# Performance work log

Hardware: AMD Instinct MI355X
Metric: run time of the kernel (lower is better)

## Reference

```python
import jax, jax.numpy as jnp
import numpy as np

INPUT_DIM = 8192
HIDDEN = 512
EMBED = HIDDEN // 2  # op embedding dim
NUM_TEMPERS = 64
NUM_OPS = 3
MAX_HOPS = 4
B = 2048


def setup_inputs() -> dict:
    key = jax.random.key(0)
    ks = jax.random.split(key, 10)
    n = lambda k, shape: jax.random.normal(k, shape, jnp.float32)
    return {
        "x": n(ks[0], (B, INPUT_DIM)),
        "op_emb": 0.01 * n(ks[1], (NUM_OPS, EMBED)),
        "op_logits": jnp.zeros((NUM_OPS,), jnp.float32),
        "id_embeds": 0.01 * n(ks[2], (128, 4)),
        "W1": n(ks[3], (HIDDEN + 4 + EMBED, HIDDEN)) / np.sqrt(HIDDEN + 4 + EMBED),
        "b1": jnp.zeros((HIDDEN,), jnp.float32),
        "W2": n(ks[4], (HIDDEN, HIDDEN)) / np.sqrt(HIDDEN),
        "b2": jnp.zeros((HIDDEN,), jnp.float32),
        "Wr1": n(ks[5], (HIDDEN + 4, 32)) / np.sqrt(HIDDEN + 4),
        "br1": jnp.zeros((32,), jnp.float32),
        "Wr2": n(ks[6], (32, NUM_TEMPERS + 1)) / np.sqrt(32),
        "br2": jnp.zeros((NUM_TEMPERS + 1,), jnp.float32),
        "Wp": n(ks[7], (HIDDEN, INPUT_DIM)) / np.sqrt(HIDDEN),
        "bp": jnp.zeros((INPUT_DIM,), jnp.float32),
        "tid_emb": 0.01 * n(ks[8], (NUM_TEMPERS, 4)),
        "rng_seed": 42,
    }


def reference(x, op_emb, op_logits, id_embeds, W1, b1, W2, b2, Wr1, br1, Wr2, br2, Wp, bp, tid_emb, rng_seed):
    Bx, D = x.shape
    # D is a multiple of HIDDEN here -> no padding branch needed
    num_patches = D // HIDDEN
    patch_states = x.reshape(Bx * num_patches, HIDDEN)
    N = patch_states.shape[0]

    rng = jax.random.key(rng_seed)
    rng, tk = jax.random.split(rng)
    patch_tempers = jax.random.randint(tk, (N,), 0, NUM_TEMPERS)
    patch_done = jnp.zeros((N,), bool)

    # Fixed-length unroll of the while_loop (max_hops=4). Early-exit only
    # differs if ALL patches stop early, which is vanishingly unlikely.
    for hop in range(MAX_HOPS):
        # --- gather active patches (inactive slots fill with index 0, as in original) ---
        active_idx = jnp.where(~patch_done, size=N, fill_value=0)[0]
        x_active = patch_states[active_idx]          # [N, HIDDEN]
        t_active = patch_tempers[active_idx]         # [N]
        # --- Temper: sample op per patch, embed, 2-layer relu MLP ---
        rng, ok = jax.random.split(rng)
        op_probs = jax.nn.softmax(op_logits)
        op_idx = jax.random.categorical(ok, jnp.log(op_probs), shape=(N,))
        x_aug = jnp.concatenate([x_active, id_embeds[t_active], op_emb[op_idx]], axis=-1)
        h = jax.nn.relu(x_aug @ W1 + b1)
        h = jax.nn.relu(h @ W2 + b2)                 # [N, HIDDEN]
        # --- scatter back updated states ---
        patch_states = patch_states.at[active_idx].set(h)
        # --- routing policy + categorical sampling of next temper / stop ---
        enriched = jnp.concatenate([h, tid_emb[t_active]], axis=-1)
        logits = jax.nn.relu(enriched @ Wr1 + br1) @ Wr2 + br2
        rng, sk = jax.random.split(rng)
        sampled = jax.random.categorical(sk, jax.nn.log_softmax(logits))
        stop = sampled == NUM_TEMPERS
        next_t = jnp.clip(sampled, 0, NUM_TEMPERS - 1)
        patch_tempers = patch_tempers.at[active_idx].set(next_t)
        patch_done = patch_done.at[active_idx].set(stop)

    latent = patch_states.reshape(Bx, num_patches, HIDDEN).mean(axis=1)  # [B, HIDDEN]
    pred = latent @ Wp + bp                                              # [B, INPUT_DIM]
    return latent, pred
```

## Files before the change

kernel.cpp:

```cpp
#include <hip/hip_runtime.h>
#include <cstdint>
#include <cstddef>


#define NPATCH 32768
#define NHOP 4
#define RSCALE 4096.0f
#define RINV   2.44140625e-4f

typedef unsigned short u16;
typedef __attribute__((ext_vector_type(8))) _Float16 half8;
typedef __attribute__((ext_vector_type(4))) float f32x4;

#define GLDS(gp, lp) __builtin_amdgcn_global_load_lds( \
    (const __attribute__((address_space(1))) void*)(const void*)(gp), \
    (__attribute__((address_space(3))) void*)(void*)(lp), 16, 0, 0)

__device__ __forceinline__ uint32_t rotl32(uint32_t x, int r){ return (x<<r)|(x>>(32-r)); }

__device__ __forceinline__ void tf2x32(uint32_t k0, uint32_t k1, uint32_t x0, uint32_t x1,
                                       uint32_t& o0, uint32_t& o1){
  uint32_t k2 = k0 ^ k1 ^ 0x1BD11BDAu;
  x0 += k0; x1 += k1;
#define TFR(r) { x0 += x1; x1 = rotl32(x1,(r)); x1 ^= x0; }
  TFR(13) TFR(15) TFR(26) TFR(6)   x0 += k1; x1 += k2 + 1u;
  TFR(17) TFR(29) TFR(16) TFR(24)  x0 += k2; x1 += k0 + 2u;
  TFR(13) TFR(15) TFR(26) TFR(6)   x0 += k0; x1 += k1 + 3u;
  TFR(17) TFR(29) TFR(16) TFR(24)  x0 += k1; x1 += k2 + 4u;
  TFR(13) TFR(15) TFR(26) TFR(6)   x0 += k2; x1 += k0 + 5u;
#undef TFR
  o0 = x0; o1 = x1;
}

__device__ __forceinline__ uint32_t jbits32(uint32_t k0, uint32_t k1, uint32_t idx){
  uint32_t a, b; tf2x32(k0, k1, 0u, idx, a, b);
  return a ^ b;
}

__device__ __forceinline__ void jsplit(uint32_t& r0, uint32_t& r1, uint32_t& c0, uint32_t& c1){
  uint32_t n0, n1;
  tf2x32(r0, r1, 0u, 0u, n0, n1);
  tf2x32(r0, r1, 0u, 1u, c0, c1);
  r0 = n0; r1 = n1;
}

__device__ __forceinline__ float jgumbel(uint32_t bits){
  float f = __uint_as_float(0x3f800000u | (bits >> 9)) - 1.0f;
  float u = fmaxf(f, 1.17549435e-38f);
  return -logf(-logf(u));
}

union uhcv { _Float16 h; u16 u; };
__device__ __forceinline__ u16 f2h(float x){ uhcv t; t.h = (_Float16)x; return t.u; }
__device__ __forceinline__ float h2f(u16 b){ uhcv t; t.u = b; return (float)t.h; }
__device__ __forceinline__ void split2s(float v, u16& a0, u16& a1){
  a0 = f2h(v);
  a1 = f2h((v - h2f(a0)) * RSCALE);
}

__global__ void k_keys(const int* __restrict__ seed, const float* __restrict__ op_logits,
                       uint32_t* __restrict__ keys, float* __restrict__ logp3){
  if (threadIdx.x != 0 || blockIdx.x != 0) return;
  uint32_t r0 = 0u, r1 = (uint32_t)seed[0];
  uint32_t c0, c1;
  jsplit(r0, r1, c0, c1); keys[0] = c0; keys[1] = c1;
  for (int h = 0; h < NHOP; h++){
    jsplit(r0, r1, c0, c1); keys[2 + 4*h] = c0; keys[3 + 4*h] = c1;
    jsplit(r0, r1, c0, c1); keys[4 + 4*h] = c0; keys[5 + 4*h] = c1;
  }
  float l0 = op_logits[0], l1 = op_logits[1], l2 = op_logits[2];
  float mm = fmaxf(l0, fmaxf(l1, l2));
  float e0 = expf(l0-mm), e1 = expf(l1-mm), e2 = expf(l2-mm);
  float ssum = e0 + e1 + e2;
  logp3[0] = logf(e0/ssum); logp3[1] = logf(e1/ssum); logp3[2] = logf(e2/ssum);
}

__global__ __launch_bounds__(256)
void k_init(const uint32_t* __restrict__ keys, int* __restrict__ tempers, int* __restrict__ done){
  int i = blockIdx.x*256 + threadIdx.x;
  uint32_t b = jbits32(keys[0], keys[1], (uint32_t)(NPATCH + i));
  tempers[i] = (int)(b & 63u);
  done[i] = 0;
}

__global__ __launch_bounds__(256)
void k_precomp(const float* __restrict__ id_embeds, const float* __restrict__ op_emb,
               const float* __restrict__ tid_emb,
               const float* __restrict__ W1, const float* __restrict__ b1,
               const float* __restrict__ Wr1, const float* __restrict__ br1,
               float* __restrict__ idW, float* __restrict__ opWb, float* __restrict__ tidWb){
  int b = blockIdx.x, tid = threadIdx.x;
  if (b < 64){
    for (int j = tid; j < 512; j += 256){
      float v = 0.f;
      #pragma unroll
      for (int u = 0; u < 4; u++) v = fmaf(id_embeds[b*4+u], W1[(size_t)(512+u)*512 + j], v);
      idW[b*512 + j] = v;
    }
  } else if (b < 67){
    int o = b - 64;
    for (int j = tid; j < 512; j += 256){
      float v = b1[j];
      for (int u = 0; u < 256; u++) v = fmaf(op_emb[o*256+u], W1[(size_t)(516+u)*512 + j], v);
      opWb[o*512 + j] = v;
    }
  } else {
    for (int idx = tid; idx < 2048; idx += 256){
      int t = idx >> 5, c = idx & 31;
      float v = br1[c];
      #pragma unroll
      for (int u = 0; u < 4; u++) v = fmaf(tid_emb[t*4+u], Wr1[(512+u)*32 + c], v);
      tidWb[idx] = v;
    }
  }
}

__global__ __launch_bounds__(256)
void k_splitW(const float* __restrict__ W1, const float* __restrict__ W2,
              const float* __restrict__ Wp, const float* __restrict__ Wr1,
              u16* __restrict__ W1T, u16* __restrict__ W2T, u16* __restrict__ WpT,
              u16* __restrict__ Wr1P){
  __shared__ float t[32][33];
  int blk = blockIdx.x;
  const float* src; u16* dst; int N; int deg; size_t pst; int tb;
  if (blk < 256){ src = W1; dst = W1T; N = 512; deg = 2; pst = (size_t)512*512; tb = blk; }
  else if (blk < 512){ src = W2; dst = W2T; N = 512; deg = 2; pst = (size_t)512*512; tb = blk - 256; }
  else if (blk < 528){ src = Wr1; dst = Wr1P; N = 32; deg = 2; pst = (size_t)32*512; tb = blk - 512; }
  else { src = Wp; dst = WpT; N = 8192; deg = 1; pst = 0; tb = blk - 528; }
  int n0 = (tb >> 4)*32, k0 = (tb & 15)*32;
  if (N == 32){ n0 = 0; k0 = tb*32; }
  int r = threadIdx.x >> 5, c = threadIdx.x & 31;
  for (int rr = r; rr < 32; rr += 8)
    t[rr][c] = src[(size_t)(k0+rr)*N + ((n0 + c) % N)];
  __syncthreads();
  for (int rr = r; rr < 32; rr += 8){
    if (n0 + rr >= N) break;
    float v = t[c][rr];
    size_t o = (size_t)(n0+rr)*512 + k0 + c;
    if (deg == 2){
      u16 a0, a1; split2s(v, a0, a1);
      dst[o] = a0; dst[pst + o] = a1;
    } else {
      dst[o] = f2h(v);
    }
  }
}

__global__ __launch_bounds__(256)
void k_xsplit(const float* __restrict__ x, u16* __restrict__ sP){
  size_t i = ((size_t)blockIdx.x*256 + threadIdx.x)*4;
  float4 v = *(const float4*)(x + i);
  ushort4 p0, p1;
  split2s(v.x, p0.x, p1.x); split2s(v.y, p0.y, p1.y);
  split2s(v.z, p0.z, p1.z); split2s(v.w, p0.w, p1.w);
  const size_t SP = (size_t)NPATCH*512;
  *(ushort4*)(sP + i) = p0; *(ushort4*)(sP + SP + i) = p1;
}

__global__ __launch_bounds__(1024)
void k_scan1(const int* __restrict__ done, int* __restrict__ lpref,
             int* __restrict__ partials){
  __shared__ int cnt[1024];
  const int tid = threadIdx.x;
  const int e = blockIdx.x*1024 + tid;
  int f = (done[e] == 0);
  cnt[tid] = f;
  __syncthreads();
  int val = f;
  for (int off = 1; off < 1024; off <<= 1){
    int v = (tid >= off) ? cnt[tid - off] : 0;
    __syncthreads();
    val += v; cnt[tid] = val;
    __syncthreads();
  }
  lpref[e] = val - f;
  if (tid == 1023) partials[blockIdx.x] = val;
}

__global__ __launch_bounds__(1024)
void k_scan3(const int* __restrict__ done, const int* __restrict__ lpref,
             const int* __restrict__ partials,
             const int* __restrict__ tempers,
             const uint32_t* __restrict__ keys, const float* __restrict__ logp3,
             int hop, int* __restrict__ aidx, int* __restrict__ t_act,
             int* __restrict__ op_idx, int* __restrict__ meta){
  __shared__ int sb[33];
  const int tid = threadIdx.x;
  if (tid < 64){
    int f = (tid < 32) ? partials[tid] : 0;
    int v = f;
    #pragma unroll
    for (int off = 1; off < 32; off <<= 1){
      int u = __shfl_up(v, off);
      if (tid >= off) v += u;
    }
    if (tid < 32) sb[tid] = v - f;
    if (tid == 31) sb[32] = v;
  }
  __syncthreads();
  const int base = sb[blockIdx.x];
  const int na = sb[32];
  const int e = blockIdx.x*1024 + tid;
  const int lp = lpref[e];
  const int f = (done[e] == 0);
  const int pos = f ? (base + lp) : (na + (e - base - lp));
  const int p = f ? e : 0;
  aidx[pos] = p;
  t_act[pos] = tempers[p];
  const uint32_t k0 = keys[2 + 4*hop], k1 = keys[3 + 4*hop];
  float best = 0.f; int bi = 0;
  #pragma unroll
  for (int c = 0; c < 3; c++){
    float v = jgumbel(jbits32(k0, k1, (uint32_t)(3*pos + c))) + logp3[c];
    if (c == 0 || v > best){ best = v; bi = c; }
  }
  op_idx[pos] = bi;
  if (blockIdx.x == 0 && tid == 0){
    meta[0] = na;
    meta[1] = (na < NPATCH) ? (NPATCH - 1) : 0;
  }
}

__global__ __launch_bounds__(1024)
void k_scan(const int* __restrict__ done, int* __restrict__ aidx, int* __restrict__ meta){
  __shared__ int cnt[1024];
  int tid = threadIdx.x;
  int base = tid * 32;
  unsigned flags = 0; int c = 0;
  #pragma unroll
  for (int i = 0; i < 32; i++){
    int f = (done[base + i] == 0);
    flags |= ((unsigned)f) << i;
    c += f;
  }
  cnt[tid] = c;
  __syncthreads();
  int val = c;
  for (int off = 1; off < 1024; off <<= 1){
    int v = (tid >= off) ? cnt[tid - off] : 0;
    __syncthreads();
    val += v; cnt[tid] = val;
    __syncthreads();
  }
  int pos = val - c;
  for (int i = 0; i < 32; i++){
    if ((flags >> i) & 1u) aidx[pos++] = base + i;
  }
  __syncthreads();
  int na = cnt[1023];
  for (int j = na + tid; j < NPATCH; j += 1024) aidx[j] = 0;
  if (tid == 0){
    meta[0] = na;
    meta[1] = (na < NPATCH) ? (NPATCH - 1) : 0;
  }
}

__global__ __launch_bounds__(256)
void k_gather(const int* __restrict__ aidx, const int* __restrict__ tempers,
              const uint32_t* __restrict__ keys, const float* __restrict__ logp3,
              int hop, int* __restrict__ t_act, int* __restrict__ op_idx){
  int s = blockIdx.x*256 + threadIdx.x;
  int p = aidx[s];
  t_act[s] = tempers[p];
  uint32_t k0 = keys[2 + 4*hop], k1 = keys[3 + 4*hop];
  float best = 0.f; int bi = 0;
  #pragma unroll
  for (int c = 0; c < 3; c++){
    float v = jgumbel(jbits32(k0, k1, (uint32_t)(3*s + c))) + logp3[c];
    if (c == 0 || v > best){ best = v; bi = c; }
  }
  op_idx[s] = bi;
}

template<int MODE, int DEG>
__global__ __launch_bounds__(256, 2)
void k_mgemm(const u16* __restrict__ Ap, const u16* __restrict__ Bp,
             float* __restrict__ outF, u16* __restrict__ outP,
             const int* __restrict__ aidx, const float* __restrict__ bias,
             const float* __restrict__ idW, const float* __restrict__ opWb,
             const int* __restrict__ t_act, const int* __restrict__ op_idx,
             const int* __restrict__ meta,
             int Ncols, size_t aStride, size_t bStride, size_t oStride){
  __shared__ u16 As[2*DEG*4096];
  __shared__ u16 Bs[2*DEG*4096];
  const int tid = threadIdx.x;
  const int L = tid & 63, w = tid >> 6;

  const int gx = (int)gridDim.x;
  const int nwg = gx * (int)gridDim.y;
  int lin = (int)blockIdx.y * gx + (int)blockIdx.x;
  if ((nwg & 7) == 0)
    lin = (lin & 7) * (nwg >> 3) + (lin >> 3);
  const int m0 = (lin / gx) * 128, n0 = (lin % gx) * 128;
  const int wr = w >> 1, wc = w & 1;

  constexpr int SPW = DEG*4;
  constexpr int BUFO = DEG*4096;
  const bool isA = (w < 2);
  const u16* gB = isA ? Ap : Bp;
  u16* lB = isA ? As : Bs;
  const size_t pstride = isA ? aStride : bStride;
  const u16* gseg[8];
  u16* lseg[8];
  #pragma unroll
  for (int q = 0; q < SPW; q++){
    int ss = (w & 1)*SPW + q;
    int p = ss >> 3, rb = ss & 7;
    int row16 = rb*16 + (L >> 2);
    int grow;
    if (isA) grow = (MODE == 1) ? aidx[m0 + row16] : (m0 + row16);
    else     grow = n0 + row16;
    int swz = (L & 3) ^ ((L >> 2) & 3);
    gseg[q] = gB + p*pstride + (size_t)grow*512 + swz*8;
    lseg[q] = lB + p*4096 + rb*512;
  }

  f32x4 accM[4][4], accR[4][4];
  #pragma unroll
  for (int i = 0; i < 4; i++)
    #pragma unroll
    for (int j = 0; j < 4; j++){ accM[i][j] = (f32x4)0.f; accR[i][j] = (f32x4)0.f; }

  const int rdsw = ((L >> 4) ^ (L & 3))*8;
  const int frow = L & 15;

  #pragma unroll
  for (int q = 0; q < SPW; q++)
    GLDS(gseg[q], lseg[q]);

  #pragma unroll 2
  for (int kt = 0; kt < 16; kt++){
    const int cb = (kt & 1) * BUFO;
    if (kt < 15){
      const int nb = ((kt + 1) & 1) * BUFO;
      #pragma unroll
      for (int q = 0; q < SPW; q++)
        GLDS(gseg[q] + (kt+1)*32, lseg[q] + nb);
      asm volatile("s_waitcnt vmcnt(%0)" :: "n"(SPW) : "memory");
    } else {
      asm volatile("s_waitcnt vmcnt(0)" ::: "memory");
    }
    __builtin_amdgcn_s_barrier();
    asm volatile("" ::: "memory");

    __builtin_amdgcn_s_setprio(1);
    half8 af[DEG][4], bf[DEG][4];
    #pragma unroll
    for (int pa = 0; pa < DEG; pa++)
      #pragma unroll
      for (int i = 0; i < 4; i++)
        af[pa][i] = *(const half8*)&As[cb + pa*4096 + (wr*64 + i*16 + frow)*32 + rdsw];
    #pragma unroll
    for (int pb = 0; pb < DEG; pb++)
      #pragma unroll
      for (int j = 0; j < 4; j++)
        bf[pb][j] = *(const half8*)&Bs[cb + pb*4096 + (wc*64 + j*16 + frow)*32 + rdsw];
    #pragma unroll
    for (int pa = 0; pa < DEG; pa++)
      #pragma unroll
      for (int pb = 0; pb < DEG - pa; pb++)
        #pragma unroll
        for (int j = 0; j < 4; j++)
          #pragma unroll
          for (int i = 0; i < 4; i++){
            if (pa + pb == 0)
              accM[i][j] = __builtin_amdgcn_mfma_f32_16x16x32_f16(af[0][i], bf[0][j], accM[i][j], 0, 0, 0);
            else
              accR[i][j] = __builtin_amdgcn_mfma_f32_16x16x32_f16(af[pa][i], bf[pb][j], accR[i][j], 0, 0, 0);
          }
    __builtin_amdgcn_s_setprio(0);

    asm volatile("" ::: "memory");
    __builtin_amdgcn_s_barrier();
  }

  const int rbase = m0 + wr*64 + (L >> 4)*4;
  const int cbase = n0 + wc*64 + (L & 15);
  const int w0v = (MODE == 3) ? meta[1] : 0;
  #pragma unroll
  for (int i = 0; i < 4; i++){
    #pragma unroll
    for (int reg = 0; reg < 4; reg++){
      int r = rbase + i*16 + reg;
      if (MODE == 1){
        int t = t_act[r], o = op_idx[r];
        #pragma unroll
        for (int j = 0; j < 4; j++){
          int c = cbase + j*16;
          float v = accM[i][j][reg] + RINV*accR[i][j][reg] + idW[t*512 + c] + opWb[o*512 + c];
          v = fmaxf(v, 0.f);
          u16 a0, a1; split2s(v, a0, a1);
          size_t off = (size_t)r*512 + c;
          outP[off] = a0; outP[oStride + off] = a1;
        }
      } else if (MODE == 3){
        int p = aidx[r];
        bool allowed = (p != 0) || (r == w0v);
        #pragma unroll
        for (int j = 0; j < 4; j++){
          int c = cbase + j*16;
          float v = accM[i][j][reg] + RINV*accR[i][j][reg] + bias[c];
          v = fmaxf(v, 0.f);
          if (allowed){
            u16 a0, a1; split2s(v, a0, a1);
            size_t off = (size_t)p*512 + c;
            outP[off] = a0; outP[oStride + off] = a1;
          }
        }
      } else {
        #pragma unroll
        for (int j = 0; j < 4; j++){
          int c = cbase + j*16;
          float v = accM[i][j][reg] + bias[c];
          if (DEG == 2) v += RINV*accR[i][j][reg];
          outF[(size_t)r*Ncols + c] = v;
        }
      }
    }
  }
}

__global__ __launch_bounds__(256)
void k_routemm(const u16* __restrict__ sP, const u16* __restrict__ Wr1P,
               const int* __restrict__ aidx, const int* __restrict__ t_act,
               const float* __restrict__ tidWb,
               const float* __restrict__ Wr2, const float* __restrict__ br2,
               const int* __restrict__ meta, const uint32_t* __restrict__ keys,
               int hop, int* __restrict__ tempers, int* __restrict__ done){
  __shared__ float l32s[64][32];
  __shared__ float Wr2s[32*65];
  const int tid = threadIdx.x;
  const int L = tid & 63, w = tid >> 6;
  const int s0 = blockIdx.x*64 + w*16;
  const size_t SPh = (size_t)NPATCH*512;

  for (int i = tid; i < 32*65; i += 256) Wr2s[i] = Wr2[i];

  const int arow = aidx[s0 + (L & 15)];
  const u16* a0p = sP + (size_t)arow*512 + (L >> 4)*8;
  const u16* a1p = a0p + SPh;
  const u16* bb = Wr1P + (size_t)(L & 15)*512 + (L >> 4)*8;
  const size_t BPL = (size_t)32*512;
  const size_t BCT = (size_t)16*512;

  f32x4 accM[2], accR[2];
  accM[0] = (f32x4)0.f; accM[1] = (f32x4)0.f;
  accR[0] = (f32x4)0.f; accR[1] = (f32x4)0.f;

  #pragma unroll 4
  for (int kt = 0; kt < 16; kt++){
    const int ko = kt*32;
    half8 a0  = *(const half8*)(a0p + ko);
    half8 a1  = *(const half8*)(a1p + ko);
    half8 b00 = *(const half8*)(bb + ko);
    half8 b01 = *(const half8*)(bb + BCT + ko);
    half8 b10 = *(const half8*)(bb + BPL + ko);
    half8 b11 = *(const half8*)(bb + BPL + BCT + ko);
    accM[0] = __builtin_amdgcn_mfma_f32_16x16x32_f16(a0, b00, accM[0], 0, 0, 0);
    accM[1] = __builtin_amdgcn_mfma_f32_16x16x32_f16(a0, b01, accM[1], 0, 0, 0);
    accR[0] = __builtin_amdgcn_mfma_f32_16x16x32_f16(a0, b10, accR[0], 0, 0, 0);
    accR[1] = __builtin_amdgcn_mfma_f32_16x16x32_f16(a0, b11, accR[1], 0, 0, 0);
    accR[0] = __builtin_amdgcn_mfma_f32_16x16x32_f16(a1, b00, accR[0], 0, 0, 0);
    accR[1] = __builtin_amdgcn_mfma_f32_16x16x32_f16(a1, b01, accR[1], 0, 0, 0);
  }

  #pragma unroll
  for (int reg = 0; reg < 4; reg++){
    int sl = w*16 + (L >> 4)*4 + reg;
    int s = blockIdx.x*64 + sl;
    int t = t_act[s];
    #pragma unroll
    for (int ct = 0; ct < 2; ct++){
      int c = ct*16 + (L & 15);
      float v = accM[ct][reg] + RINV*accR[ct][reg] + tidWb[t*32 + c];
      l32s[sl][c] = fmaxf(v, 0.f);
    }
  }
  __syncthreads();

  const uint32_t sk0 = keys[4 + 4*hop], sk1 = keys[5 + 4*hop];
  const int w0v = meta[1];
  for (int rr = 0; rr < 16; rr++){
    const int sl = w*16 + rr;
    const int ps = blockIdx.x*64 + sl;
    const int c = L;
    float lg = br2[c];
    #pragma unroll
    for (int k = 0; k < 32; k++) lg = fmaf(l32s[sl][k], Wr2s[k*65 + c], lg);
    float lg64 = br2[64];
    #pragma unroll
    for (int k = 0; k < 32; k++) lg64 = fmaf(l32s[sl][k], Wr2s[k*65 + 64], lg64);
    float m = lg;
    for (int off = 32; off; off >>= 1) m = fmaxf(m, __shfl_xor(m, off));
    m = fmaxf(m, lg64);
    float se = expf(lg - m);
    for (int off = 32; off; off >>= 1) se += __shfl_xor(se, off);
    se += expf(lg64 - m);
    float Lse = logf(se);
    float g = jgumbel(jbits32(sk0, sk1, (uint32_t)(65*ps + c)));
    float v = (lg - m) - Lse + g;
    int idx = c;
    for (int off = 32; off; off >>= 1){
      float ov = __shfl_xor(v, off);
      int   oi = __shfl_xor(idx, off);
      if (ov > v || (ov == v && oi < idx)){ v = ov; idx = oi; }
    }
    float g64 = jgumbel(jbits32(sk0, sk1, (uint32_t)(65*ps + 64)));
    float v64 = (lg64 - m) - Lse + g64;
    if (v64 > v) idx = 64;
    if (L == 0){
      const int p = aidx[ps];
      const bool allowed = (p != 0) || (ps == w0v);
      if (allowed){
        tempers[p] = (idx < 63) ? idx : 63;
        done[p]    = (idx == 64) ? 1 : 0;
      }
    }
  }
}

__global__ __launch_bounds__(256)
void k_latent2(const u16* __restrict__ sP, float* __restrict__ outF, u16* __restrict__ latP){
  int idx = blockIdx.x*256 + threadIdx.x;
  int b = idx >> 7, j4 = (idx & 127)*4;
  const size_t SP = (size_t)NPATCH*512;
  float s0 = 0.f, s1 = 0.f, s2 = 0.f, s3 = 0.f;
  #pragma unroll 4
  for (int u = 0; u < 16; u++){
    size_t e = (size_t)(b*16 + u)*512 + j4;
    ushort4 v0 = *(const ushort4*)(sP + e);
    ushort4 v1 = *(const ushort4*)(sP + SP + e);
    s0 += h2f(v0.x) + RINV*h2f(v1.x);
    s1 += h2f(v0.y) + RINV*h2f(v1.y);
    s2 += h2f(v0.z) + RINV*h2f(v1.z);
    s3 += h2f(v0.w) + RINV*h2f(v1.w);
  }
  s0 *= 0.0625f; s1 *= 0.0625f; s2 *= 0.0625f; s3 *= 0.0625f;
  float4 fo; fo.x = s0; fo.y = s1; fo.z = s2; fo.w = s3;
  *(float4*)(outF + (size_t)b*512 + j4) = fo;
  ushort4 lp; lp.x = f2h(s0); lp.y = f2h(s1); lp.z = f2h(s2); lp.w = f2h(s3);
  *(ushort4*)(latP + (size_t)b*512 + j4) = lp;
}

template<int MODE>
__global__ __launch_bounds__(256)
void k_gemmF(const float* __restrict__ A, const float* __restrict__ B, float* __restrict__ C,
             int Ncols,
             const int* __restrict__ aidx,
             const float* __restrict__ bias,
             const float* __restrict__ idW, const float* __restrict__ opWb,
             const int* __restrict__ t_act, const int* __restrict__ op_idx){
  __shared__ float As[16][128];
  __shared__ float Bs[16][128];
  const int tid = threadIdx.x;
  const int bx = blockIdx.x, by = blockIdx.y;
  const int tx = tid & 15, ty = tid >> 4;
  const int lr = tid >> 1, lhalf = tid & 1;
  const int srow = by*128 + lr;
  const int arow = (MODE == 1) ? aidx[srow] : srow;
  const float* Ap = A + (size_t)arow*512 + lhalf*8;
  const float* Bp = B + (size_t)(tid >> 4)*Ncols + bx*128 + (tid & 15)*8;

  float acc[8][8];
  #pragma unroll
  for (int i = 0; i < 8; i++)
    #pragma unroll
    for (int j = 0; j < 8; j++) acc[i][j] = 0.f;

  for (int kt = 0; kt < 512; kt += 16){
    float4 a0 = *(const float4*)(Ap + kt);
    float4 a1 = *(const float4*)(Ap + kt + 4);
    float4 g0 = *(const float4*)(Bp + (size_t)kt*Ncols);
    float4 g1 = *(const float4*)(Bp + (size_t)kt*Ncols + 4);
    __syncthreads();
    As[lhalf*8+0][lr] = a0.x; As[lhalf*8+1][lr] = a0.y;
    As[lhalf*8+2][lr] = a0.z; As[lhalf*8+3][lr] = a0.w;
    As[lhalf*8+4][lr] = a1.x; As[lhalf*8+5][lr] = a1.y;
    As[lhalf*8+6][lr] = a1.z; As[lhalf*8+7][lr] = a1.w;
    *(float4*)&Bs[tid>>4][(tid&15)*8]     = g0;
    *(float4*)&Bs[tid>>4][(tid&15)*8 + 4] = g1;
    __syncthreads();
    #pragma unroll
    for (int k = 0; k < 16; k++){
      float4 av0 = *(float4*)&As[k][ty*8];
      float4 av1 = *(float4*)&As[k][ty*8+4];
      float4 bv0 = *(float4*)&Bs[k][tx*4];
      float4 bv1 = *(float4*)&Bs[k][64 + tx*4];
      float av[8] = {av0.x,av0.y,av0.z,av0.w,av1.x,av1.y,av1.z,av1.w};
      float bv[8] = {bv0.x,bv0.y,bv0.z,bv0.w,bv1.x,bv1.y,bv1.z,bv1.w};
      #pragma unroll
      for (int i = 0; i < 8; i++)
        #pragma unroll
        for (int j = 0; j < 8; j++)
          acc[i][j] = fmaf(av[i], bv[j], acc[i][j]);
    }
  }

  const int col0a = bx*128 + tx*4;
  const int col0b = col0a + 64;
  #pragma unroll
  for (int i = 0; i < 8; i++){
    int s = by*128 + ty*8 + i;
    float adda[4], addb[4];
    if (MODE == 1){
      int t = t_act[s], o = op_idx[s];
      float4 ia = *(const float4*)&idW[t*512 + col0a];
      float4 ib = *(const float4*)&idW[t*512 + col0b];
      float4 oa = *(const float4*)&opWb[o*512 + col0a];
      float4 ob = *(const float4*)&opWb[o*512 + col0b];
      adda[0]=ia.x+oa.x; adda[1]=ia.y+oa.y; adda[2]=ia.z+oa.z; adda[3]=ia.w+oa.w;
      addb[0]=ib.x+ob.x; addb[1]=ib.y+ob.y; addb[2]=ib.z+ob.z; addb[3]=ib.w+ob.w;
    } else {
      float4 ba = *(const float4*)&bias[col0a];
      float4 bb = *(const float4*)&bias[col0b];
      adda[0]=ba.x; adda[1]=ba.y; adda[2]=ba.z; adda[3]=ba.w;
      addb[0]=bb.x; addb[1]=bb.y; addb[2]=bb.z; addb[3]=bb.w;
    }
    float4 va, vb;
    float* pa = &va.x; float* pb = &vb.x;
    #pragma unroll
    for (int j = 0; j < 4; j++){
      float v0 = acc[i][j]   + adda[j];
      float v1 = acc[i][j+4] + addb[j];
      if (MODE != 2){ v0 = fmaxf(v0, 0.f); v1 = fmaxf(v1, 0.f); }
      pa[j] = v0; pb[j] = v1;
    }
    *(float4*)(C + (size_t)s*Ncols + col0a) = va;
    *(float4*)(C + (size_t)s*Ncols + col0b) = vb;
  }
}

__global__ __launch_bounds__(256)
void k_routeF(const float* __restrict__ h2, const float* __restrict__ Wr1,
              const float* __restrict__ Wr2, const float* __restrict__ br2,
              const float* __restrict__ tidWb,
              const int* __restrict__ t_act, const int* __restrict__ aidx,
              const int* __restrict__ meta, const uint32_t* __restrict__ keys, int hop,
              float* __restrict__ states, int* __restrict__ tempers, int* __restrict__ done){
  __shared__ float Wr1s[256][32];
  __shared__ float h2s[8][512];
  __shared__ float l32[8][32];

  const int tid = threadIdx.x;
  const int s0 = blockIdx.x * 8;

  for (int i4 = tid; i4 < 8*128; i4 += 256){
    int sl = i4 >> 7, q = i4 & 127;
    *(float4*)&h2s[sl][q*4] = *(const float4*)&h2[(size_t)(s0+sl)*512 + q*4];
  }

  const int lane = tid & 63, w = tid >> 6;
  const int half = lane >> 5, col = lane & 31;
  const int sl = w*2 + half;
  const int s  = s0 + sl;
  const int t  = t_act[s];
  float acc = tidWb[t*32 + col];

  for (int kh = 0; kh < 2; kh++){
    __syncthreads();
    for (int idx = tid; idx < 256*32; idx += 256)
      Wr1s[idx >> 5][idx & 31] = Wr1[kh*8192 + idx];
    __syncthreads();
    const int kb = kh * 256;
    #pragma unroll 4
    for (int k4 = 0; k4 < 64; k4++){
      float4 hv = *(float4*)&h2s[sl][kb + k4*4];
      acc = fmaf(hv.x, Wr1s[k4*4+0][col], acc);
      acc = fmaf(hv.y, Wr1s[k4*4+1][col], acc);
      acc = fmaf(hv.z, Wr1s[k4*4+2][col], acc);
      acc = fmaf(hv.w, Wr1s[k4*4+3][col], acc);
    }
  }
  l32[sl][col] = fmaxf(acc, 0.f);
  __syncthreads();

  const uint32_t sk0 = keys[4 + 4*hop], sk1 = keys[5 + 4*hop];
  int smp[2];
  for (int pass = 0; pass < 2; pass++){
    const int psl = w*2 + pass;
    const int ps  = s0 + psl;
    const int c = lane;
    float lg = br2[c];
    #pragma unroll
    for (int k = 0; k < 32; k++) lg = fmaf(l32[psl][k], Wr2[k*65 + c], lg);
    float lg64 = br2[64];
    #pragma unroll
    for (int k = 0; k < 32; k++) lg64 = fmaf(l32[psl][k], Wr2[k*65 + 64], lg64);
    float m = lg;
    for (int off = 32; off; off >>= 1) m = fmaxf(m, __shfl_xor(m, off));
    m = fmaxf(m, lg64);
    float se = expf(lg - m);
    for (int off = 32; off; off >>= 1) se += __shfl_xor(se, off);
    se += expf(lg64 - m);
    float Lse = logf(se);
    float g = jgumbel(jbits32(sk0, sk1, (uint32_t)(65*ps + c)));
    float v = (lg - m) - Lse + g;
    int idx = c;
    for (int off = 32; off; off >>= 1){
      float ov = __shfl_xor(v, off);
      int   oi = __shfl_xor(idx, off);
      if (ov > v || (ov == v && oi < idx)){ v = ov; idx = oi; }
    }
    float g64 = jgumbel(jbits32(sk0, sk1, (uint32_t)(65*ps + 64)));
    float v64 = (lg64 - m) - Lse + g64;
    if (v64 > v) idx = 64;
    smp[pass] = idx;
  }

  const int mysmp = smp[half];
  const int p = aidx[s];
  const int w0v = meta[1];
  const bool allowed = (p != 0) || (s == w0v);
  if (allowed){
    const float4* src = (const float4*)&h2s[sl][0];
    float4* dst = (float4*)(states + (size_t)p*512);
    for (int q = col; q < 128; q += 32) dst[q] = src[q];
    if (col == 0){
      tempers[p] = (mysmp < 63) ? mysmp : 63;
      done[p]    = (mysmp == 64) ? 1 : 0;
    }
  }
}

__global__ __launch_bounds__(256)
void k_latentF(const float* __restrict__ states, float* __restrict__ out){
  int idx = blockIdx.x*256 + threadIdx.x;
  int b = idx >> 9, j = idx & 511;
  float s = 0.f;
  #pragma unroll
  for (int u = 0; u < 16; u++) s += states[(size_t)(b*16 + u)*512 + j];
  out[idx] = s * 0.0625f;
}

extern "C" void kernel_launch(void* const* d_in, const int* in_sizes, int n_in,
                              void* d_out, int out_size, void* d_ws, size_t ws_size,
                              hipStream_t stream) {
  (void)in_sizes; (void)n_in; (void)out_size;
  const float* x         = (const float*)d_in[0];
  const float* op_emb    = (const float*)d_in[1];
  const float* op_logits = (const float*)d_in[2];
  const float* id_embeds = (const float*)d_in[3];
  const float* W1        = (const float*)d_in[4];
  const float* b1        = (const float*)d_in[5];
  const float* W2        = (const float*)d_in[6];
  const float* b2        = (const float*)d_in[7];
  const float* Wr1       = (const float*)d_in[8];
  const float* br1       = (const float*)d_in[9];
  const float* Wr2       = (const float*)d_in[10];
  const float* br2       = (const float*)d_in[11];
  const float* Wp        = (const float*)d_in[12];
  const float* bp        = (const float*)d_in[13];
  const float* tid_emb   = (const float*)d_in[14];
  const int*   seed      = (const int*)d_in[15];
  float* out = (float*)d_out;

  char* w = (char*)d_ws;
  uint32_t* keys = (uint32_t*)w;
  float* logp3   = (float*)(w + 256);
  int*   meta    = (int*)(w + 512);
  int*   tempers = (int*)(w + 4096);
  int*   done    = tempers + NPATCH;
  int*   t_act   = done + NPATCH;
  int*   op_idx  = t_act + NPATCH;
  int*   aidx    = op_idx + NPATCH;
  int*   lpref   = aidx + NPATCH;
  float* idW     = (float*)(lpref + NPATCH);
  float* opWb    = idW + 64*512;
  float* tidWb   = opWb + 3*512;
  int*   partials= (int*)(tidWb + 2048);

  const size_t SPh = (size_t)NPATCH*512;
  u16* W1T     = (u16*)(w + (1u<<20));
  u16* W2T     = W1T + (size_t)2*512*512;
  u16* Wr1P    = W2T + (size_t)2*512*512;
  u16* WpT     = Wr1P + (size_t)2*32*512;
  u16* latP    = WpT + (size_t)8192*512;
  u16* statesP = latP + (size_t)2048*512;
  u16* h1P     = statesP + 2*SPh;
  const size_t NEED = (size_t)((char*)(h1P + 2*SPh) - w);

  k_keys<<<1, 64, 0, stream>>>(seed, op_logits, keys, logp3);
  k_init<<<NPATCH/256, 256, 0, stream>>>(keys, tempers, done);
  k_precomp<<<68, 256, 0, stream>>>(id_embeds, op_emb, tid_emb, W1, b1, Wr1, br1,
                                    idW, opWb, tidWb);

  if (ws_size >= NEED){
    k_splitW<<<4624, 256, 0, stream>>>(W1, W2, Wp, Wr1, W1T, W2T, WpT, Wr1P);
    k_xsplit<<<(NPATCH*512/4)/256, 256, 0, stream>>>(x, statesP);

    for (int hop = 0; hop < NHOP; hop++){
      k_scan1<<<NPATCH/1024, 1024, 0, stream>>>(done, lpref, partials);
      k_scan3<<<NPATCH/1024, 1024, 0, stream>>>(done, lpref, partials,
                                                tempers, keys, logp3, hop,
                                                aidx, t_act, op_idx, meta);
      k_mgemm<1,2><<<dim3(4, NPATCH/128), 256, 0, stream>>>(
          statesP, W1T, nullptr, h1P, aidx, nullptr, idW, opWb, t_act, op_idx, meta,
          512, SPh, (size_t)512*512, SPh);
      k_mgemm<3,2><<<dim3(4, NPATCH/128), 256, 0, stream>>>(
          h1P, W2T, nullptr, statesP, aidx, b2, nullptr, nullptr, nullptr, nullptr, meta,
          512, SPh, (size_t)512*512, SPh);
      k_routemm<<<NPATCH/64, 256, 0, stream>>>(statesP, Wr1P, aidx, t_act, tidWb,
                                               Wr2, br2, meta, keys, hop,
                                               tempers, done);
    }

    k_latent2<<<(2048*512/4)/256, 256, 0, stream>>>(statesP, out, latP);
    k_mgemm<2,1><<<dim3(64, 16), 256, 0, stream>>>(
        latP, WpT, out + 2048*512, nullptr, nullptr, bp, nullptr, nullptr, nullptr, nullptr,
        nullptr, 8192, (size_t)2048*512, (size_t)8192*512, 0);
  } else {
    const size_t BIG0 = 2u<<20;
    const size_t SB   = (size_t)NPATCH * 512 * sizeof(float);
    float *states, *h1, *h2;
    bool copy_states;
    if (ws_size >= BIG0 + 3*SB){
      states = (float*)(w + BIG0);
      h1     = (float*)(w + BIG0 + SB);
      h2     = (float*)(w + BIG0 + 2*SB);
      copy_states = true;
    } else {
      states = (float*)d_in[0];
      h1     = (float*)(w + BIG0);
      h2     = (float*)(w + BIG0 + SB);
      copy_states = false;
    }
    if (copy_states)
      hipMemcpyAsync(states, x, SB, hipMemcpyDeviceToDevice, stream);

    for (int hop = 0; hop < NHOP; hop++){
      k_scan<<<1, 1024, 0, stream>>>(done, aidx, meta);
      k_gather<<<NPATCH/256, 256, 0, stream>>>(aidx, tempers, keys, logp3, hop, t_act, op_idx);
      k_gemmF<1><<<dim3(4, NPATCH/128), 256, 0, stream>>>(states, W1, h1, 512,
                                      aidx, nullptr, idW, opWb, t_act, op_idx);
      k_gemmF<0><<<dim3(4, NPATCH/128), 256, 0, stream>>>(h1, W2, h2, 512,
                                      nullptr, b2, nullptr, nullptr, nullptr, nullptr);
      k_routeF<<<NPATCH/8, 256, 0, stream>>>(h2, Wr1, Wr2, br2, tidWb, t_act, aidx,
                                      meta, keys, hop, states, tempers, done);
    }

    k_latentF<<<(2048*512)/256, 256, 0, stream>>>(states, out);
    k_gemmF<2><<<dim3(8192/128, 2048/128), 256, 0, stream>>>(out, Wp, out + 2048*512, 8192,
                                      nullptr, bp, nullptr, nullptr, nullptr, nullptr);
  }
}
```

Before: 986.0 us.

## Add split-precision GEMM kernel with four-slot half-tile LDS pipeline

Adds a dedicated k_mgemmP kernel for the two per-hop split-fp16 GEMMs. It stages the high and low halves of each K tile into separate LDS slots in a four-deep ring, so loads of the next half overlap with MFMAs on the current one, with a barrier at each half-step. It also restructures fragment reads in the remaining generic k_mgemm to load B fragments per column, reducing register pressure. The aim is to hide global-to-LDS latency and raise MFMA utilisation, at the cost of more barriers and hand-tuned vmcnt waits that must stay matched to the number of loads issued.

```diff
diff --git a/kernel.cpp b/kernel.cpp
--- a/kernel.cpp
+++ b/kernel.cpp
@@ -272,6 +272,157 @@
   op_idx[s] = bi;
 }
 
+template<int MODE>
+__global__ __launch_bounds__(256, 2)
+void k_mgemmP(const u16* __restrict__ Ap, const u16* __restrict__ Bp,
+              u16* __restrict__ outP,
+              const int* __restrict__ aidx, const float* __restrict__ bias,
+              const float* __restrict__ idW, const float* __restrict__ opWb,
+              const int* __restrict__ t_act, const int* __restrict__ op_idx,
+              const int* __restrict__ meta,
+              size_t aStride, size_t bStride, size_t oStride){
+  __shared__ u16 As[4*4096];
+  __shared__ u16 Bs[4*4096];
+  const int tid = threadIdx.x;
+  const int L = tid & 63, w = tid >> 6;
+
+  const int gx = (int)gridDim.x;
+  const int nwg = gx * (int)gridDim.y;
+  int lin = (int)blockIdx.y * gx + (int)blockIdx.x;
+  if ((nwg & 7) == 0)
+    lin = (lin & 7) * (nwg >> 3) + (lin >> 3);
+  const int m0 = (lin / gx) * 128, n0 = (lin % gx) * 128;
+  const int wr = w >> 1, wc = w & 1;
+
+  const int swz = (L & 3) ^ ((L >> 2) & 3);
+  const int row16 = L >> 2;
+  const u16* gA[2][2];
+  const u16* gB[2][2];
+  int lofs[2];
+  #pragma unroll
+  for (int q = 0; q < 2; q++){
+    const int rb = 2*w + q;
+    lofs[q] = rb*512;
+    int growA = m0 + rb*16 + row16;
+    if (MODE == 1) growA = aidx[growA];
+    const int growB = n0 + rb*16 + row16;
+    #pragma unroll
+    for (int p = 0; p < 2; p++){
+      gA[p][q] = Ap + p*aStride + (size_t)growA*512 + swz*8;
+      gB[p][q] = Bp + p*bStride + (size_t)growB*512 + swz*8;
+    }
+  }
+
+#define ISSUE_HALF(t, p) { const int _sl = ((2*(t)+(p)) & 3)*4096; \
+    GLDS(gA[p][0] + (t)*32, As + _sl + lofs[0]); \
+    GLDS(gA[p][1] + (t)*32, As + _sl + lofs[1]); \
+    GLDS(gB[p][0] + (t)*32, Bs + _sl + lofs[0]); \
+    GLDS(gB[p][1] + (t)*32, Bs + _sl + lofs[1]); }
+
+  f32x4 accM[4][4], accR[4][4];
+  #pragma unroll
+  for (int i = 0; i < 4; i++)
+    #pragma unroll
+    for (int j = 0; j < 4; j++){ accM[i][j] = (f32x4)0.f; accR[i][j] = (f32x4)0.f; }
+
+  const int rdsw = ((L >> 4) ^ (L & 3))*8;
+  const int frow = L & 15;
+
+#define READ_FRAGS(dA, dB, sl) { \
+    const int _b = (sl)*4096; \
+    dA[0] = *(const half8*)&As[_b + (wr*64 +  0 + frow)*32 + rdsw]; \
+    dA[1] = *(const half8*)&As[_b + (wr*64 + 16 + frow)*32 + rdsw]; \
+    dA[2] = *(const half8*)&As[_b + (wr*64 + 32 + frow)*32 + rdsw]; \
+    dA[3] = *(const half8*)&As[_b + (wr*64 + 48 + frow)*32 + rdsw]; \
+    dB[0] = *(const half8*)&Bs[_b + (wc*64 +  0 + frow)*32 + rdsw]; \
+    dB[1] = *(const half8*)&Bs[_b + (wc*64 + 16 + frow)*32 + rdsw]; \
+    dB[2] = *(const half8*)&Bs[_b + (wc*64 + 32 + frow)*32 + rdsw]; \
+    dB[3] = *(const half8*)&Bs[_b + (wc*64 + 48 + frow)*32 + rdsw]; }
+
+#define MFMA_CL(dst, aa, bb) { \
+    _Pragma("unroll") \
+    for (int j = 0; j < 4; j++) \
+      _Pragma("unroll") \
+      for (int i = 0; i < 4; i++) \
+        dst[i][j] = __builtin_amdgcn_mfma_f32_16x16x32_f16(aa[i], bb[j], dst[i][j], 0, 0, 0); }
+
+  ISSUE_HALF(0, 0); ISSUE_HALF(0, 1); ISSUE_HALF(1, 0);
+
+  half8 af0[4], bf0[4], af1[4], bf1[4];
+
+  for (int t = 0; t < 15; t++){
+    asm volatile("s_waitcnt vmcnt(8)" ::: "memory");
+    __builtin_amdgcn_s_barrier();
+    asm volatile("" ::: "memory");
+    ISSUE_HALF(t+1, 1);
+    READ_FRAGS(af0, bf0, (2*t) & 3);
+    __builtin_amdgcn_s_setprio(1);
+    MFMA_CL(accM, af0, bf0);
+    __builtin_amdgcn_s_setprio(0);
+    asm volatile("s_waitcnt vmcnt(8)" ::: "memory");
+    __builtin_amdgcn_s_barrier();
+    asm volatile("" ::: "memory");
+    if (t < 14) ISSUE_HALF(t+2, 0);
+    READ_FRAGS(af1, bf1, (2*t+1) & 3);
+    __builtin_amdgcn_s_setprio(1);
+    MFMA_CL(accR, af0, bf1);
+    MFMA_CL(accR, af1, bf0);
+    __builtin_amdgcn_s_setprio(0);
+  }
+  asm volatile("s_waitcnt vmcnt(4)" ::: "memory");
+  __builtin_amdgcn_s_barrier();
+  asm volatile("" ::: "memory");
+  READ_FRAGS(af0, bf0, 2);
+  MFMA_CL(accM, af0, bf0);
+  asm volatile("s_waitcnt vmcnt(0)" ::: "memory");
+  __builtin_amdgcn_s_barrier();
+  asm volatile("" ::: "memory");
+  READ_FRAGS(af1, bf1, 3);
+  MFMA_CL(accR, af0, bf1);
+  MFMA_CL(accR, af1, bf0);
+
+#undef ISSUE_HALF
+#undef READ_FRAGS
+#undef MFMA_CL
+
+  const int rbase = m0 + wr*64 + (L >> 4)*4;
+  const int cbase = n0 + wc*64 + (L & 15);
+  const int w0v = (MODE == 3) ? meta[1] : 0;
+  #pragma unroll
+  for (int i = 0; i < 4; i++){
+    #pragma unroll
+    for (int reg = 0; reg < 4; reg++){
+      int r = rbase + i*16 + reg;
+      if (MODE == 1){
+        int t = t_act[r], o = op_idx[r];
+        #pragma unroll
+        for (int j = 0; j < 4; j++){
+          int c = cbase + j*16;
+          float v = accM[i][j][reg] + RINV*accR[i][j][reg] + idW[t*512 + c] + opWb[o*512 + c];
+          v = fmaxf(v, 0.f);
+          u16 a0, a1; split2s(v, a0, a1);
+          size_t off = (size_t)r*512 + c;
+          outP[off] = a0; outP[oStride + off] = a1;
+        }
+      } else {
+        int p = aidx[r];
+        bool allowed = (p != 0) || (r == w0v);
+        #pragma unroll
+        for (int j = 0; j < 4; j++){
+          int c = cbase + j*16;
+          float v = accM[i][j][reg] + RINV*accR[i][j][reg] + bias[c];
+          v = fmaxf(v, 0.f);
+          if (allowed){
+            u16 a0, a1; split2s(v, a0, a1);
+            size_t off = (size_t)p*512 + c;
+            outP[off] = a0; outP[oStride + off] = a1;
+          }
+        }
+      }
+    }
+  }
+}
+
 template<int MODE, int DEG>
 __global__ __launch_bounds__(256, 2)
 void k_mgemm(const u16* __restrict__ Ap, const u16* __restrict__ Bp,
@@ -344,30 +495,27 @@
     asm volatile("" ::: "memory");
 
     __builtin_amdgcn_s_setprio(1);
-    half8 af[DEG][4], bf[DEG][4];
-    #pragma unroll
-    for (int pa = 0; pa < DEG; pa++)
+    #pragma unroll
+    for (int pa = 0; pa < DEG; pa++){
+      half8 af[4];
       #pragma unroll
       for (int i = 0; i < 4; i++)
-        af[pa][i] = *(const half8*)&As[cb + pa*4096 + (wr*64 + i*16 + frow)*32 + rdsw];
-    #pragma unroll
-    for (int pb = 0; pb < DEG; pb++)
+        af[i] = *(const half8*)&As[cb + pa*4096 + (wr*64 + i*16 + frow)*32 + rdsw];
       #pragma unroll
-      for (int j = 0; j < 4; j++)
-        bf[pb][j] = *(const half8*)&Bs[cb + pb*4096 + (wc*64 + j*16 + frow)*32 + rdsw];
-    #pragma unroll
-    for (int pa = 0; pa < DEG; pa++)
-      #pragma unroll
-      for (int pb = 0; pb < DEG - pa; pb++)
+      for (int pb = 0; pb < DEG - pa; pb++){
         #pragma unroll
-        for (int j = 0; j < 4; j++)
+        for (int j = 0; j < 4; j++){
+          half8 bf = *(const half8*)&Bs[cb + pb*4096 + (wc*64 + j*16 + frow)*32 + rdsw];
           #pragma unroll
           for (int i = 0; i < 4; i++){
             if (pa + pb == 0)
-              accM[i][j] = __builtin_amdgcn_mfma_f32_16x16x32_f16(af[0][i], bf[0][j], accM[i][j], 0, 0, 0);
+              accM[i][j] = __builtin_amdgcn_mfma_f32_16x16x32_f16(af[i], bf, accM[i][j], 0, 0, 0);
             else
-              accR[i][j] = __builtin_amdgcn_mfma_f32_16x16x32_f16(af[pa][i], bf[pb][j], accR[i][j], 0, 0, 0);
+              accR[i][j] = __builtin_amdgcn_mfma_f32_16x16x32_f16(af[i], bf, accR[i][j], 0, 0, 0);
           }
+        }
+      }
+    }
     __builtin_amdgcn_s_setprio(0);
 
     asm volatile("" ::: "memory");
@@ -376,45 +524,17 @@
 
   const int rbase = m0 + wr*64 + (L >> 4)*4;
   const int cbase = n0 + wc*64 + (L & 15);
-  const int w0v = (MODE == 3) ? meta[1] : 0;
   #pragma unroll
   for (int i = 0; i < 4; i++){
     #pragma unroll
     for (int reg = 0; reg < 4; reg++){
       int r = rbase + i*16 + reg;
-      if (MODE == 1){
-        int t = t_act[r], o = op_idx[r];
-        #pragma unroll
-        for (int j = 0; j < 4; j++){
-          int c = cbase + j*16;
-          float v = accM[i][j][reg] + RINV*accR[i][j][reg] + idW[t*512 + c] + opWb[o*512 + c];
-          v = fmaxf(v, 0.f);
-          u16 a0, a1; split2s(v, a0, a1);
-          size_t off = (size_t)r*512 + c;
-          outP[off] = a0; outP[oStride + off] = a1;
-        }
-      } else if (MODE == 3){
-        int p = aidx[r];
-        bool allowed = (p != 0) || (r == w0v);
-        #pragma unroll
-        for (int j = 0; j < 4; j++){
-          int c = cbase + j*16;
-          float v = accM[i][j][reg] + RINV*accR[i][j][reg] + bias[c];
-          v = fmaxf(v, 0.f);
-          if (allowed){
-            u16 a0, a1; split2s(v, a0, a1);
-            size_t off = (size_t)p*512 + c;
-            outP[off] = a0; outP[oStride + off] = a1;
-          }
-        }
-      } else {
-        #pragma unroll
-        for (int j = 0; j < 4; j++){
-          int c = cbase + j*16;
-          float v = accM[i][j][reg] + bias[c];
-          if (DEG == 2) v += RINV*accR[i][j][reg];
-          outF[(size_t)r*Ncols + c] = v;
-        }
+      #pragma unroll
+      for (int j = 0; j < 4; j++){
+        int c = cbase + j*16;
+        float v = accM[i][j][reg] + bias[c];
+        if (DEG == 2) v += RINV*accR[i][j][reg];
+        outF[(size_t)r*Ncols + c] = v;
       }
     }
   }
@@ -793,12 +913,12 @@
       k_scan3<<<NPATCH/1024, 1024, 0, stream>>>(done, lpref, partials,
                                                 tempers, keys, logp3, hop,
                                                 aidx, t_act, op_idx, meta);
-      k_mgemm<1,2><<<dim3(4, NPATCH/128), 256, 0, stream>>>(
-          statesP, W1T, nullptr, h1P, aidx, nullptr, idW, opWb, t_act, op_idx, meta,
-          512, SPh, (size_t)512*512, SPh);
-      k_mgemm<3,2><<<dim3(4, NPATCH/128), 256, 0, stream>>>(
-          h1P, W2T, nullptr, statesP, aidx, b2, nullptr, nullptr, nullptr, nullptr, meta,
-          512, SPh, (size_t)512*512, SPh);
+      k_mgemmP<1><<<dim3(4, NPATCH/128), 256, 0, stream>>>(
+          statesP, W1T, h1P, aidx, nullptr, idW, opWb, t_act, op_idx, meta,
+          SPh, (size_t)512*512, SPh);
+      k_mgemmP<3><<<dim3(4, NPATCH/128), 256, 0, stream>>>(
+          h1P, W2T, statesP, aidx, b2, nullptr, nullptr, nullptr, nullptr, meta,
+          SPh, (size_t)512*512, SPh);
       k_routemm<<<NPATCH/64, 256, 0, stream>>>(statesP, Wr1P, aidx, t_act, tidWb,
                                                Wr2, br2, meta, keys, hop,
                                                tempers, done);
```

Result: slower. 1.023 ms (+3.8%).
